# Kernel optimization log

Measured on AMD Instinct MI355X. Metric: run time of the kernel, lower is better.

The kernel has to match this reference:

```python
import jax, jax.numpy as jnp
import numpy as np
from jax.scipy.special import gammaln, digamma, polygamma

B, K = 8192, 128
LAMBDA_KL = 1.0
LAMBDA_LOGDET = 0.01
JITTER = 1e-6


def setup_inputs() -> dict:
    key = jax.random.key(0)
    k1, k2 = jax.random.split(key)
    # Dirichlet concentrations must be > 0
    alpha = jax.random.uniform(k1, (B, K), jnp.float32, 0.5, 5.0)
    target = jax.random.randint(k2, (B,), 0, K)
    return {"alpha": alpha, "target": target}


def _fisher_diag(alpha):
    # trigamma(alpha_i) - trigamma(S)
    s = alpha.sum(axis=1, keepdims=True)
    return polygamma(1, alpha) - polygamma(1, s)


def reference(alpha, target):
    bsz, k = alpha.shape
    dtype = alpha.dtype
    s = alpha.sum(axis=1, keepdims=True)          # [B,1]
    y = jax.nn.one_hot(target, k, dtype=dtype)    # [B,K]

    # ---- i_mse (Fisher-weighted Brier) ----
    p = alpha / s
    err = (y - p) ** 2
    var = p * (1.0 - p) / (s + 1.0)
    w = jnp.clip(_fisher_diag(alpha), 1e-8)       # clamp_min
    i_mse = (w * (err + var)).sum(axis=1).mean()

    # ---- KL( Dir(alpha_hat) || Dir(1) ) ----
    alpha_hat = alpha * (1.0 - y) + y             # evidence removed at true class
    s_hat = alpha_hat.sum(axis=1)                 # [B]
    kl_ps = (gammaln(s_hat)
             - gammaln(jnp.asarray(float(k), dtype))
             - gammaln(alpha_hat).sum(axis=1)
             + ((alpha_hat - 1.0)
                * (digamma(alpha_hat) - digamma(s_hat)[:, None])).sum(axis=1))
    kl = kl_ps.mean()

    # ---- log|FIM|, FIM = diag(trigamma(alpha)) - trigamma(S) * 11^T ----
    trig = polygamma(1, alpha)                    # [B,K]
    trig_s = polygamma(1, alpha.sum(axis=1))      # [B]
    eye = jnp.eye(k, dtype=dtype)
    fim = trig[:, :, None] * eye - trig_s[:, None, None] + JITTER * eye  # [B,K,K]
    sign, logabsdet = jnp.linalg.slogdet(fim)
    logdet_ps = jnp.where(sign > 0, logabsdet, jnp.full_like(logabsdet, -20.0))
    logdet_mean = logdet_ps.mean()

    total = i_mse + LAMBDA_KL * kl - LAMBDA_LOGDET * logdet_mean
    return (total, i_mse, kl, logdet_mean)
```

## Files before the change

kernel.cpp:

```cpp
#include <hip/hip_runtime.h>
#include <hip/hip_bf16.h>
#include <math.h>

#define B_ROWS   8192
#define K_DIM    128
#define NBLOCKS  1024
#define NTHREADS 512
#define NWAVES   8
#define JITTER   1e-6f

__device__ __forceinline__ float rcpf(float x) { return __builtin_amdgcn_rcpf(x); }

__device__ __forceinline__ void special3(float x, float& dg, float& tg, float& lg) {
    const float x1 = x + 1.f, x2 = x + 2.f, x3 = x + 3.f, x4 = x + 4.f, x5 = x + 5.f;
    const float r0 = rcpf(x),  r1 = rcpf(x1), r2 = rcpf(x2);
    const float r3 = rcpf(x3), r4 = rcpf(x4), r5 = rcpf(x5);
    const float y  = x + 6.f;
    const float iy = rcpf(y);
    const float f  = iy * iy;
    const float ly = __logf(y);

    const float dg_y = ly - 0.5f * iy
                     + f * (-1.f/12.f + f * (1.f/120.f + f * (-1.f/252.f)));
    dg = dg_y - (((r0 + r1) + (r2 + r3)) + (r4 + r5));

    const float tg_y = iy * (1.f + iy * (0.5f + iy * (1.f/6.f
                     + f * (-1.f/30.f + f * (1.f/42.f)))));
    tg = tg_y + (((r0*r0 + r1*r1) + (r2*r2 + r3*r3)) + (r4*r4 + r5*r5));

    const float lg_y = (y - 0.5f) * ly - y + 0.91893853320467274f
                     + iy * (1.f/12.f + f * (-1.f/360.f + f * (1.f/1260.f)));
    const float prod = ((x * x1) * (x2 * x3)) * (x4 * x5);
    lg = lg_y - __logf(prod);
}

__device__ __forceinline__ float digamma_big(float y) {
    const float iy = rcpf(y), f = iy * iy;
    return __logf(y) - 0.5f * iy - f * (1.f/12.f);
}
__device__ __forceinline__ float trigamma_big(float y) {
    const float iy = rcpf(y), f = iy * iy;
    return iy + 0.5f * f + f * iy * (1.f/6.f);
}
__device__ __forceinline__ float lgamma_big(float y) {
    const float iy = rcpf(y);
    return (y - 0.5f) * __logf(y) - y + 0.91893853320467274f + iy * (1.f/12.f);
}

__global__ __launch_bounds__(NTHREADS)
void iedl_rows(const float* __restrict__ alpha,
               const int* __restrict__ target,
               float* __restrict__ ws) {
    const int wave = threadIdx.x >> 6;
    const int lane = threadIdx.x & 63;
    const int b    = blockIdx.x * NWAVES + wave;

    const float2 a2 = ((const float2*)(alpha + (size_t)b * K_DIM))[lane];
    const int tgt = target[b];

    float s = a2.x + a2.y;
    #pragma unroll
    for (int m = 1; m < 64; m <<= 1) s += __shfl_xor(s, m);

    const float a_pick = (tgt & 1) ? a2.y : a2.x;
    const float a_t    = __shfl(a_pick, tgt >> 1);

    const float s_hat  = s - a_t + 1.f;
    const float trig_s = trigamma_big(s);
    const float dg_sh  = digamma_big(s_hat);
    const float inv_s  = rcpf(s);
    const float inv_s1 = rcpf(s + 1.f);

    float mse_sum = 0.f, kl_sum = 0.f, logd_sum = 0.f, invd_sum = 0.f;
    #pragma unroll
    for (int e = 0; e < 2; ++e) {
        const int   k  = 2 * lane + e;
        const float ad = (e == 0) ? a2.x : a2.y;

        float dg_a, tg_a, lg_a;
        special3(ad, dg_a, tg_a, lg_a);

        const float p   = ad * inv_s;
        const float y1  = (k == tgt) ? 1.f : 0.f;
        const float err = (y1 - p) * (y1 - p);
        const float var = p * (1.f - p) * inv_s1;
        const float w   = fmaxf(tg_a - trig_s, 1e-8f);
        mse_sum += w * (err + var);

        if (k != tgt) kl_sum += -lg_a + (ad - 1.f) * (dg_a - dg_sh);

        const float D = tg_a + JITTER;
        logd_sum += __logf(D);
        invd_sum += rcpf(D);
    }

    #pragma unroll
    for (int m = 1; m < 64; m <<= 1) {
        mse_sum  += __shfl_xor(mse_sum,  m);
        kl_sum   += __shfl_xor(kl_sum,   m);
        logd_sum += __shfl_xor(logd_sum, m);
        invd_sum += __shfl_xor(invd_sum, m);
    }

    const float acc_kl = lgamma_big(s_hat) - 491.5534482f + kl_sum;
    const float t      = 1.f - trig_s * invd_sum;
    const float acc_ld = (t > 0.f) ? (logd_sum + __logf(t)) : -20.f;

    __shared__ float sm[3][NWAVES];
    if (lane == 0) { sm[0][wave] = mse_sum; sm[1][wave] = acc_kl; sm[2][wave] = acc_ld; }
    __syncthreads();

    if (threadIdx.x == 0) {
        float M = 0.f, KK = 0.f, L = 0.f;
        #pragma unroll
        for (int w = 0; w < NWAVES; ++w) { M += sm[0][w]; KK += sm[1][w]; L += sm[2][w]; }
        ws[blockIdx.x]               = M;
        ws[NBLOCKS + blockIdx.x]     = KK;
        ws[2 * NBLOCKS + blockIdx.x] = L;
    }
}

__global__ __launch_bounds__(256)
void iedl_reduce(const float* __restrict__ ws, float* __restrict__ out) {
    const int tid  = threadIdx.x;
    const int wave = tid >> 6;
    const int lane = tid & 63;

    const float4 m4 = ((const float4*)(ws))[tid];
    const float4 k4 = ((const float4*)(ws + NBLOCKS))[tid];
    const float4 l4 = ((const float4*)(ws + 2 * NBLOCKS))[tid];

    double m = ((double)m4.x + (double)m4.y) + ((double)m4.z + (double)m4.w);
    double k = ((double)k4.x + (double)k4.y) + ((double)k4.z + (double)k4.w);
    double l = ((double)l4.x + (double)l4.y) + ((double)l4.z + (double)l4.w);

    #pragma unroll
    for (int off = 1; off < 64; off <<= 1) {
        m += __shfl_xor(m, off);
        k += __shfl_xor(k, off);
        l += __shfl_xor(l, off);
    }

    __shared__ double sm[3][4];
    if (lane == 0) { sm[0][wave] = m; sm[1][wave] = k; sm[2][wave] = l; }
    __syncthreads();

    if (tid == 0) {
        double M = 0.0, KK = 0.0, L = 0.0;
        #pragma unroll
        for (int w = 0; w < 4; ++w) { M += sm[0][w]; KK += sm[1][w]; L += sm[2][w]; }
        const double inv_b = 1.0 / (double)B_ROWS;
        const double i_mse = M * inv_b;
        const double kl    = KK * inv_b;
        const double ldm   = L * inv_b;
        out[0] = (float)(i_mse + kl - 0.01 * ldm);
        out[1] = (float)i_mse;
        out[2] = (float)kl;
        out[3] = (float)ldm;
    }
}

extern "C" void kernel_launch(void* const* d_in, const int* in_sizes, int n_in,
                              void* d_out, int out_size, void* d_ws, size_t ws_size,
                              hipStream_t stream) {
    const float* alpha  = (const float*)d_in[0];
    const int*   target = (const int*)d_in[1];
    float*       out    = (float*)d_out;
    float*       ws     = (float*)d_ws;

    iedl_rows<<<NBLOCKS, NTHREADS, 0, stream>>>(alpha, target, ws);
    iedl_reduce<<<1, 256, 0, stream>>>(ws, out);
}
```

Measured before the change: 61.42 us.

## Fuse final reduction via last-block atomic counter and pack two rows per wave

Merges the per-row kernel and the final reduction kernel into a single launch. Each block bumps a global atomic counter, and the last block to finish performs the double-precision reduction. Each wave now handles two rows, with every lane loading a float4, which halves the threads per block and doubles the per-thread special-function work while keeping the block count at 1024. This removes one kernel launch and its dependency gap, at the cost of an atomic and extra fence and sync work in every block.

```diff
diff --git a/kernel.cpp b/kernel.cpp
--- a/kernel.cpp
+++ b/kernel.cpp
@@ -1,13 +1,14 @@
 #include <hip/hip_runtime.h>
-#include <hip/hip_bf16.h>
 #include <math.h>
 
 #define B_ROWS   8192
 #define K_DIM    128
 #define NBLOCKS  1024
-#define NTHREADS 512
-#define NWAVES   8
+#define NTHREADS 256
+#define NWAVES   4
 #define JITTER   1e-6f
+
+__device__ int g_cnt = 0;
 
 __device__ __forceinline__ float rcpf(float x) { return __builtin_amdgcn_rcpf(x); }
 
@@ -48,22 +49,26 @@
 }
 
 __global__ __launch_bounds__(NTHREADS)
-void iedl_rows(const float* __restrict__ alpha,
-               const int* __restrict__ target,
-               float* __restrict__ ws) {
+void iedl_fused(const float* __restrict__ alpha,
+                const int* __restrict__ target,
+                float* __restrict__ ws,
+                float* __restrict__ out) {
     const int wave = threadIdx.x >> 6;
     const int lane = threadIdx.x & 63;
-    const int b    = blockIdx.x * NWAVES + wave;
-
-    const float2 a2 = ((const float2*)(alpha + (size_t)b * K_DIM))[lane];
+    const int hl   = lane & 31;
+    const int half = lane >> 5;
+    const int b    = blockIdx.x * (NWAVES * 2) + wave * 2 + half;
+
+    const float4 a4 = ((const float4*)(alpha + (size_t)b * K_DIM))[hl];
     const int tgt = target[b];
 
-    float s = a2.x + a2.y;
-    #pragma unroll
-    for (int m = 1; m < 64; m <<= 1) s += __shfl_xor(s, m);
-
-    const float a_pick = (tgt & 1) ? a2.y : a2.x;
-    const float a_t    = __shfl(a_pick, tgt >> 1);
+    float s = (a4.x + a4.y) + (a4.z + a4.w);
+    #pragma unroll
+    for (int m = 1; m < 32; m <<= 1) s += __shfl_xor(s, m);
+
+    const int   te   = tgt & 3;
+    const float pick = (te == 0) ? a4.x : (te == 1) ? a4.y : (te == 2) ? a4.z : a4.w;
+    const float a_t  = __shfl(pick, (lane & 32) + (tgt >> 2));
 
     const float s_hat  = s - a_t + 1.f;
     const float trig_s = trigamma_big(s);
@@ -71,11 +76,13 @@
     const float inv_s  = rcpf(s);
     const float inv_s1 = rcpf(s + 1.f);
 
-    float mse_sum = 0.f, kl_sum = 0.f, logd_sum = 0.f, invd_sum = 0.f;
-    #pragma unroll
-    for (int e = 0; e < 2; ++e) {
-        const int   k  = 2 * lane + e;
-        const float ad = (e == 0) ? a2.x : a2.y;
+    const float ae[4] = {a4.x, a4.y, a4.z, a4.w};
+    float mse_a = 0.f, mse_b = 0.f, kl_a = 0.f, kl_b = 0.f;
+    float ld_a  = 0.f, ld_b  = 0.f, iv_a = 0.f, iv_b = 0.f;
+    #pragma unroll
+    for (int e = 0; e < 4; ++e) {
+        const int   k  = 4 * hl + e;
+        const float ad = ae[e];
 
         float dg_a, tg_a, lg_a;
         special3(ad, dg_a, tg_a, lg_a);
@@ -85,17 +92,23 @@
         const float err = (y1 - p) * (y1 - p);
         const float var = p * (1.f - p) * inv_s1;
         const float w   = fmaxf(tg_a - trig_s, 1e-8f);
-        mse_sum += w * (err + var);
-
-        if (k != tgt) kl_sum += -lg_a + (ad - 1.f) * (dg_a - dg_sh);
-
-        const float D = tg_a + JITTER;
-        logd_sum += __logf(D);
-        invd_sum += rcpf(D);
-    }
-
-    #pragma unroll
-    for (int m = 1; m < 64; m <<= 1) {
+        const float mt  = w * (err + var);
+
+        const float D  = tg_a + JITTER;
+        const float lt = __logf(D);
+        const float it = rcpf(D);
+        const float kt = (k != tgt) ? (-lg_a + (ad - 1.f) * (dg_a - dg_sh)) : 0.f;
+
+        if (e < 2) { mse_a += mt; kl_a += kt; ld_a += lt; iv_a += it; }
+        else       { mse_b += mt; kl_b += kt; ld_b += lt; iv_b += it; }
+    }
+
+    float mse_sum  = mse_a + mse_b;
+    float kl_sum   = kl_a  + kl_b;
+    float logd_sum = ld_a  + ld_b;
+    float invd_sum = iv_a  + iv_b;
+    #pragma unroll
+    for (int m = 1; m < 32; m <<= 1) {
         mse_sum  += __shfl_xor(mse_sum,  m);
         kl_sum   += __shfl_xor(kl_sum,   m);
         logd_sum += __shfl_xor(logd_sum, m);
@@ -106,25 +119,43 @@
     const float t      = 1.f - trig_s * invd_sum;
     const float acc_ld = (t > 0.f) ? (logd_sum + __logf(t)) : -20.f;
 
-    __shared__ float sm[3][NWAVES];
-    if (lane == 0) { sm[0][wave] = mse_sum; sm[1][wave] = acc_kl; sm[2][wave] = acc_ld; }
+    __shared__ float smp[3][NWAVES][2];
+    __shared__ int   last_flag;
+    if (hl == 0) {
+        smp[0][wave][half] = mse_sum;
+        smp[1][wave][half] = acc_kl;
+        smp[2][wave][half] = acc_ld;
+    }
     __syncthreads();
 
     if (threadIdx.x == 0) {
         float M = 0.f, KK = 0.f, L = 0.f;
         #pragma unroll
-        for (int w = 0; w < NWAVES; ++w) { M += sm[0][w]; KK += sm[1][w]; L += sm[2][w]; }
+        for (int w = 0; w < NWAVES; ++w) {
+            M  += smp[0][w][0]; M  += smp[0][w][1];
+            KK += smp[1][w][0]; KK += smp[1][w][1];
+            L  += smp[2][w][0]; L  += smp[2][w][1];
+        }
         ws[blockIdx.x]               = M;
         ws[NBLOCKS + blockIdx.x]     = KK;
         ws[2 * NBLOCKS + blockIdx.x] = L;
-    }
-}
-
-__global__ __launch_bounds__(256)
-void iedl_reduce(const float* __restrict__ ws, float* __restrict__ out) {
+
+        const int old = __hip_atomic_fetch_add(&g_cnt, 1, __ATOMIC_ACQ_REL,
+                                               __HIP_MEMORY_SCOPE_AGENT);
+        const int last = (old == NBLOCKS - 1);
+        if (last) {
+            __hip_atomic_store(&g_cnt, 0, __ATOMIC_RELAXED,
+                               __HIP_MEMORY_SCOPE_AGENT);
+            __threadfence();
+        }
+        last_flag = last;
+    }
+    __syncthreads();
+    if (!last_flag) return;
+
     const int tid  = threadIdx.x;
-    const int wave = tid >> 6;
-    const int lane = tid & 63;
+    const int rwav = tid >> 6;
+    const int rlan = tid & 63;
 
     const float4 m4 = ((const float4*)(ws))[tid];
     const float4 k4 = ((const float4*)(ws + NBLOCKS))[tid];
@@ -141,14 +172,14 @@
         l += __shfl_xor(l, off);
     }
 
-    __shared__ double sm[3][4];
-    if (lane == 0) { sm[0][wave] = m; sm[1][wave] = k; sm[2][wave] = l; }
+    __shared__ double smd[3][4];
+    if (rlan == 0) { smd[0][rwav] = m; smd[1][rwav] = k; smd[2][rwav] = l; }
     __syncthreads();
 
     if (tid == 0) {
         double M = 0.0, KK = 0.0, L = 0.0;
         #pragma unroll
-        for (int w = 0; w < 4; ++w) { M += sm[0][w]; KK += sm[1][w]; L += sm[2][w]; }
+        for (int w = 0; w < 4; ++w) { M += smd[0][w]; KK += smd[1][w]; L += smd[2][w]; }
         const double inv_b = 1.0 / (double)B_ROWS;
         const double i_mse = M * inv_b;
         const double kl    = KK * inv_b;
@@ -168,6 +199,5 @@
     float*       out    = (float*)d_out;
     float*       ws     = (float*)d_ws;
 
-    iedl_rows<<<NBLOCKS, NTHREADS, 0, stream>>>(alpha, target, ws);
-    iedl_reduce<<<1, 256, 0, stream>>>(ws, out);
-}
+    iedl_fused<<<NBLOCKS, NTHREADS, 0, stream>>>(alpha, target, ws, out);
+}
```

Measured after the change: 80.65 us. 31.3% more time.
